# Performance work log

Hardware: AMD Instinct MI355X
Metric: run time of the kernel (lower is better)

The kernel has to match this reference:

```python
import jax, jax.numpy as jnp
import numpy as np

B, C_FEATS, T = 8, 256, 1024
NUM_COMP = 64
EPS = 1e-9


def setup_inputs() -> dict:
    key = jax.random.key(0)
    k1, k2 = jax.random.split(key)
    x = jax.random.normal(k1, (B, C_FEATS, T), dtype=jnp.float32)
    mu = jax.random.normal(k2, (NUM_COMP, C_FEATS), dtype=jnp.float32)
    prec = jnp.ones((NUM_COMP,), dtype=jnp.float32)
    return {"x": x, "mu": mu, "prec": prec}


def reference(x, mu, prec):
    # x: (B, F, T) -> (B, T, F), matching torch transpose(1, -1)
    xt = jnp.swapaxes(x, 1, 2)
    # squared distance to each centroid via expansion (avoids (B,T,C,F) delta):
    x2 = jnp.sum(xt * xt, axis=-1, keepdims=True)            # (B, T, 1)
    mu2 = jnp.sum(mu * mu, axis=-1)                           # (C,)
    xmu = jnp.einsum('btf,cf->btc', xt, mu)                   # (B, T, C)
    dist = x2 - 2.0 * xmu + mu2                               # (B, T, C)
    llk = -(prec * prec) * dist                               # use_bias=False
    r = jax.nn.softmax(llk, axis=-1)                          # (B, T, C)
    Nraw = jnp.sum(r, axis=1)                                 # (B, C)
    N = Nraw + EPS
    # F = sum_t r*(x - mu) = sum_t r*x - (sum_t r)*mu
    F = jnp.einsum('btc,btf->bcf', r, xt) - Nraw[..., None] * mu  # (B, C, F)
    pool = F / N[..., None]
    return pool.reshape(x.shape[0], -1)                       # (B, C*F)
```

## Files before the change

kernel.cpp:

```cpp
#include <hip/hip_runtime.h>

#define BB 8
#define FF 256
#define TT 1024
#define CC 64
constexpr float EPS = 1e-9f;

#define TCHUNK 16
#define NTILE 64
#define BT 64
#define NTQ 16
#define BCF (BB * CC * FF)

#define WS_R   0
#define WS_NP  524288
#define WS_FP  557056

__global__ __launch_bounds__(256) void passA_kernel(const float* __restrict__ x,
                                                    const float* __restrict__ mu,
                                                    const float* __restrict__ prec,
                                                    float* __restrict__ ws) {
    __shared__ __align__(16) float xt[TCHUNK][260];
    __shared__ __align__(16) float Sred[4][TCHUNK][68];
    __shared__ __align__(16) float rl[TCHUNK][68];
    __shared__ float x2s[TCHUNK];
    __shared__ float mu2s[CC], p2s[CC];

    const int tid = threadIdx.x;
    const int b    = blockIdx.x >> 6;
    const int tile = blockIdx.x & 63;
    const int t0   = tile * TCHUNK;
    const float* xb = x + (size_t)b * FF * TT;

    {
        const int c = tid >> 2, q = tid & 3;
        const float* mp = mu + c * FF + q * 64;
        float s = 0.f;
        #pragma unroll
        for (int i = 0; i < 16; ++i) {
            float4 v = *(const float4*)(mp + i * 4);
            s += v.x * v.x + v.y * v.y + v.z * v.z + v.w * v.w;
        }
        s += __shfl_xor(s, 1);
        s += __shfl_xor(s, 2);
        if (q == 0) mu2s[c] = s;
        if (tid < CC) { float p = prec[tid]; p2s[tid] = p * p; }
    }

    #pragma unroll
    for (int i = 0; i < 4; ++i) {
        const int id = i * 256 + tid;
        const int f = id >> 2, seg = id & 3;
        float4 v = *(const float4*)(xb + f * TT + t0 + seg * 4);
        xt[seg * 4 + 0][f] = v.x;
        xt[seg * 4 + 1][f] = v.y;
        xt[seg * 4 + 2][f] = v.z;
        xt[seg * 4 + 3][f] = v.w;
    }
    __syncthreads();

    {
        const int t = tid >> 4, kk = tid & 15;
        float s = 0.f;
        #pragma unroll
        for (int q = 0; q < 16; ++q) { float v = xt[t][kk + 16 * q]; s += v * v; }
        s += __shfl_xor(s, 1);
        s += __shfl_xor(s, 2);
        s += __shfl_xor(s, 4);
        s += __shfl_xor(s, 8);
        if (kk == 0) x2s[t] = s;
    }
    __syncthreads();

    {
        const int g = tid >> 6;
        const int lane = tid & 63;
        const int tr = lane & 7;
        const int c0 = (lane >> 3) * 8;
        float acc[2][8];
        #pragma unroll
        for (int i = 0; i < 2; ++i)
            #pragma unroll
            for (int j = 0; j < 8; ++j) acc[i][j] = 0.f;

        const float* mupt = mu + (size_t)c0 * FF + g * 64;
        #pragma unroll 4
        for (int kk = 0; kk < 16; ++kk) {
            const int f4 = g * 64 + kk * 4;
            float4 xv0 = *(const float4*)&xt[tr][f4];
            float4 xv1 = *(const float4*)&xt[tr + 8][f4];
            #pragma unroll
            for (int j = 0; j < 8; ++j) {
                float4 mv = *(const float4*)(mupt + j * FF + kk * 4);
                acc[0][j] += xv0.x * mv.x + xv0.y * mv.y + xv0.z * mv.z + xv0.w * mv.w;
                acc[1][j] += xv1.x * mv.x + xv1.y * mv.y + xv1.z * mv.z + xv1.w * mv.w;
            }
        }
        #pragma unroll
        for (int i = 0; i < 2; ++i) {
            *(float4*)&Sred[g][tr + 8 * i][c0] =
                make_float4(acc[i][0], acc[i][1], acc[i][2], acc[i][3]);
            *(float4*)&Sred[g][tr + 8 * i][c0 + 4] =
                make_float4(acc[i][4], acc[i][5], acc[i][6], acc[i][7]);
        }
    }
    __syncthreads();

    {
        const int t = tid >> 4, kk = tid & 15;
        const int c4 = kk * 4;
        float Sx = 0.f, Sy = 0.f, Sz = 0.f, Sw = 0.f;
        #pragma unroll
        for (int gg = 0; gg < 4; ++gg) {
            float4 v = *(const float4*)&Sred[gg][t][c4];
            Sx += v.x; Sy += v.y; Sz += v.z; Sw += v.w;
        }
        const float x2v = x2s[t];
        float l0 = -p2s[c4 + 0] * (x2v - 2.f * Sx + mu2s[c4 + 0]);
        float l1 = -p2s[c4 + 1] * (x2v - 2.f * Sy + mu2s[c4 + 1]);
        float l2 = -p2s[c4 + 2] * (x2v - 2.f * Sz + mu2s[c4 + 2]);
        float l3 = -p2s[c4 + 3] * (x2v - 2.f * Sw + mu2s[c4 + 3]);
        float m = fmaxf(fmaxf(l0, l1), fmaxf(l2, l3));
        m = fmaxf(m, __shfl_xor(m, 1));
        m = fmaxf(m, __shfl_xor(m, 2));
        m = fmaxf(m, __shfl_xor(m, 4));
        m = fmaxf(m, __shfl_xor(m, 8));
        float e0 = __expf(l0 - m), e1 = __expf(l1 - m);
        float e2 = __expf(l2 - m), e3 = __expf(l3 - m);
        float sum = e0 + e1 + e2 + e3;
        sum += __shfl_xor(sum, 1);
        sum += __shfl_xor(sum, 2);
        sum += __shfl_xor(sum, 4);
        sum += __shfl_xor(sum, 8);
        const float inv = 1.f / sum;
        *(float4*)&rl[t][c4] = make_float4(e0 * inv, e1 * inv, e2 * inv, e3 * inv);
    }
    __syncthreads();

    if (tid < CC) {
        float ns = 0.f;
        #pragma unroll
        for (int t = 0; t < TCHUNK; ++t) ns += rl[t][tid];
        ws[WS_NP + (size_t)blockIdx.x * CC + tid] = ns;
    }

    {
        const int c = tid >> 2, seg = tid & 3;
        float4 v;
        v.x = rl[seg * 4 + 0][c];
        v.y = rl[seg * 4 + 1][c];
        v.z = rl[seg * 4 + 2][c];
        v.w = rl[seg * 4 + 3][c];
        *(float4*)(ws + WS_R + ((size_t)b * CC + c) * TT + t0 + seg * 4) = v;
    }
}

__global__ __launch_bounds__(256) void passB_kernel(const float* __restrict__ x,
                                                    float* __restrict__ ws) {
    __shared__ __align__(16) float xs[BT][68];
    __shared__ __align__(16) float rs[CC][68];
    const int tid = threadIdx.x;
    const int bid = blockIdx.x;
    const int b   = bid >> 6;
    const int fsl = (bid >> 4) & 3;
    const int tq  = bid & 15;
    const int f0  = fsl * 64;
    const int t0  = tq * BT;
    const float* xb = x + (size_t)b * FF * TT;
    const float* rb = ws + WS_R + (size_t)b * CC * TT;

    #pragma unroll
    for (int it = 0; it < 4; ++it) {
        const int id = it * 256 + tid;
        {
            const int ff = id >> 4, seg = id & 15;
            float4 v = *(const float4*)(xb + (f0 + ff) * TT + t0 + seg * 4);
            xs[seg * 4 + 0][ff] = v.x;
            xs[seg * 4 + 1][ff] = v.y;
            xs[seg * 4 + 2][ff] = v.z;
            xs[seg * 4 + 3][ff] = v.w;
        }
        {
            const int c = id >> 4, cs = id & 15;
            float4 v = *(const float4*)(rb + (size_t)c * TT + t0 + cs * 4);
            *(float4*)&rs[c][cs * 4] = v;
        }
    }
    __syncthreads();

    const int fi = tid & 15, cg = tid >> 4;
    float acc[4][4];
    #pragma unroll
    for (int j = 0; j < 4; ++j)
        #pragma unroll
        for (int e = 0; e < 4; ++e) acc[j][e] = 0.f;

    #pragma unroll 8
    for (int t = 0; t < BT; ++t) {
        float4 xv = *(const float4*)&xs[t][fi * 4];
        #pragma unroll
        for (int j = 0; j < 4; ++j) {
            float rv = rs[cg * 4 + j][t];
            acc[j][0] += rv * xv.x;
            acc[j][1] += rv * xv.y;
            acc[j][2] += rv * xv.z;
            acc[j][3] += rv * xv.w;
        }
    }

    float* fp = ws + WS_FP + (size_t)tq * BCF + (size_t)b * CC * FF;
    #pragma unroll
    for (int j = 0; j < 4; ++j)
        *(float4*)(fp + (cg * 4 + j) * FF + f0 + fi * 4) =
            make_float4(acc[j][0], acc[j][1], acc[j][2], acc[j][3]);
}

__global__ __launch_bounds__(256) void final_kernel(const float* __restrict__ mu,
                                                    const float* __restrict__ ws,
                                                    float* __restrict__ out) {
    const int b = blockIdx.x >> 6, c = blockIdx.x & 63;
    const int f = threadIdx.x;
    float nr = 0.f;
    const float* np = ws + WS_NP + (size_t)b * NTILE * CC + c;
    #pragma unroll
    for (int tile = 0; tile < NTILE; ++tile) nr += np[tile * CC];
    const float* fp = ws + WS_FP + (size_t)b * CC * FF + c * FF + f;
    float s = 0.f;
    #pragma unroll
    for (int p = 0; p < NTQ; ++p) s += fp[(size_t)p * BCF];
    out[((size_t)b * CC + c) * FF + f] = (s - nr * mu[c * FF + f]) / (nr + EPS);
}

extern "C" void kernel_launch(void* const* d_in, const int* in_sizes, int n_in,
                              void* d_out, int out_size, void* d_ws, size_t ws_size,
                              hipStream_t stream) {
    const float* x    = (const float*)d_in[0];
    const float* mu   = (const float*)d_in[1];
    const float* prec = (const float*)d_in[2];
    float* out = (float*)d_out;
    float* ws  = (float*)d_ws;

    passA_kernel<<<512, 256, 0, stream>>>(x, mu, prec, ws);
    passB_kernel<<<512, 256, 0, stream>>>(x, ws);
    final_kernel<<<512, 256, 0, stream>>>(mu, ws, out);
}
```

Baseline: 33.44 us.

## Restructure phase-1 distance GEMV without cross-group reduction; transpose r tile in phase 2

Phase 1 now gives each thread one timestep and four centroids and runs over all 256 features. It computes x^2 inline, which removes the Sred cross-group reduction buffer, the separate x2 pass and two barriers. The cost is that every thread streams its own mu rows from global memory and runs a longer serial loop with less ILP. Phase 2 stores the responsibility tile transposed in shared memory, so the inner loop reads one float4 of r per timestep instead of four scalar loads. This adds strided scalar LDS writes during the fill.

```diff
diff --git a/kernel.cpp b/kernel.cpp
--- a/kernel.cpp
+++ b/kernel.cpp
@@ -6,30 +6,26 @@
 #define CC 64
 constexpr float EPS = 1e-9f;
 
-#define TCHUNK 16
-#define NTILE 64
 #define BT 64
 #define NTQ 16
+#define NTILE 64
 #define BCF (BB * CC * FF)
 
 #define WS_R   0
 #define WS_NP  524288
 #define WS_FP  557056
 
-__global__ __launch_bounds__(256) void passA_kernel(const float* __restrict__ x,
-                                                    const float* __restrict__ mu,
-                                                    const float* __restrict__ prec,
-                                                    float* __restrict__ ws) {
-    __shared__ __align__(16) float xt[TCHUNK][260];
-    __shared__ __align__(16) float Sred[4][TCHUNK][68];
-    __shared__ __align__(16) float rl[TCHUNK][68];
-    __shared__ float x2s[TCHUNK];
+__global__ __launch_bounds__(256, 4) void k_phase1(
+        const float* __restrict__ x, const float* __restrict__ mu,
+        const float* __restrict__ prec, float* __restrict__ ws) {
+    __shared__ __align__(16) float xt[16][260];
+    __shared__ __align__(16) float rl[16][68];
     __shared__ float mu2s[CC], p2s[CC];
 
     const int tid = threadIdx.x;
     const int b    = blockIdx.x >> 6;
     const int tile = blockIdx.x & 63;
-    const int t0   = tile * TCHUNK;
+    const int t0   = tile * 16;
     const float* xb = x + (size_t)b * FF * TT;
 
     {
@@ -48,8 +44,8 @@
     }
 
     #pragma unroll
-    for (int i = 0; i < 4; ++i) {
-        const int id = i * 256 + tid;
+    for (int it = 0; it < 4; ++it) {
+        const int id = it * 256 + tid;
         const int f = id >> 2, seg = id & 3;
         float4 v = *(const float4*)(xb + f * TT + t0 + seg * 4);
         xt[seg * 4 + 0][f] = v.x;
@@ -60,66 +56,28 @@
     __syncthreads();
 
     {
-        const int t = tid >> 4, kk = tid & 15;
-        float s = 0.f;
-        #pragma unroll
-        for (int q = 0; q < 16; ++q) { float v = xt[t][kk + 16 * q]; s += v * v; }
-        s += __shfl_xor(s, 1);
-        s += __shfl_xor(s, 2);
-        s += __shfl_xor(s, 4);
-        s += __shfl_xor(s, 8);
-        if (kk == 0) x2s[t] = s;
-    }
-    __syncthreads();
-
-    {
-        const int g = tid >> 6;
-        const int lane = tid & 63;
-        const int tr = lane & 7;
-        const int c0 = (lane >> 3) * 8;
-        float acc[2][8];
-        #pragma unroll
-        for (int i = 0; i < 2; ++i)
-            #pragma unroll
-            for (int j = 0; j < 8; ++j) acc[i][j] = 0.f;
-
-        const float* mupt = mu + (size_t)c0 * FF + g * 64;
+        const int tc = tid & 15, tg = tid >> 4;
+        const int c4 = tc * 4;
+        float acc0 = 0.f, acc1 = 0.f, acc2 = 0.f, acc3 = 0.f, x2v = 0.f;
+        const float* mup = mu + (size_t)c4 * FF;
         #pragma unroll 4
-        for (int kk = 0; kk < 16; ++kk) {
-            const int f4 = g * 64 + kk * 4;
-            float4 xv0 = *(const float4*)&xt[tr][f4];
-            float4 xv1 = *(const float4*)&xt[tr + 8][f4];
-            #pragma unroll
-            for (int j = 0; j < 8; ++j) {
-                float4 mv = *(const float4*)(mupt + j * FF + kk * 4);
-                acc[0][j] += xv0.x * mv.x + xv0.y * mv.y + xv0.z * mv.z + xv0.w * mv.w;
-                acc[1][j] += xv1.x * mv.x + xv1.y * mv.y + xv1.z * mv.z + xv1.w * mv.w;
-            }
-        }
-        #pragma unroll
-        for (int i = 0; i < 2; ++i) {
-            *(float4*)&Sred[g][tr + 8 * i][c0] =
-                make_float4(acc[i][0], acc[i][1], acc[i][2], acc[i][3]);
-            *(float4*)&Sred[g][tr + 8 * i][c0 + 4] =
-                make_float4(acc[i][4], acc[i][5], acc[i][6], acc[i][7]);
-        }
-    }
-    __syncthreads();
-
-    {
-        const int t = tid >> 4, kk = tid & 15;
-        const int c4 = kk * 4;
-        float Sx = 0.f, Sy = 0.f, Sz = 0.f, Sw = 0.f;
-        #pragma unroll
-        for (int gg = 0; gg < 4; ++gg) {
-            float4 v = *(const float4*)&Sred[gg][t][c4];
-            Sx += v.x; Sy += v.y; Sz += v.z; Sw += v.w;
-        }
-        const float x2v = x2s[t];
-        float l0 = -p2s[c4 + 0] * (x2v - 2.f * Sx + mu2s[c4 + 0]);
-        float l1 = -p2s[c4 + 1] * (x2v - 2.f * Sy + mu2s[c4 + 1]);
-        float l2 = -p2s[c4 + 2] * (x2v - 2.f * Sz + mu2s[c4 + 2]);
-        float l3 = -p2s[c4 + 3] * (x2v - 2.f * Sw + mu2s[c4 + 3]);
+        for (int kk = 0; kk < 64; ++kk) {
+            float4 xv = *(const float4*)&xt[tg][kk * 4];
+            x2v += xv.x * xv.x + xv.y * xv.y + xv.z * xv.z + xv.w * xv.w;
+            float4 m0 = *(const float4*)(mup + 0 * FF + kk * 4);
+            float4 m1 = *(const float4*)(mup + 1 * FF + kk * 4);
+            float4 m2 = *(const float4*)(mup + 2 * FF + kk * 4);
+            float4 m3 = *(const float4*)(mup + 3 * FF + kk * 4);
+            acc0 += xv.x * m0.x + xv.y * m0.y + xv.z * m0.z + xv.w * m0.w;
+            acc1 += xv.x * m1.x + xv.y * m1.y + xv.z * m1.z + xv.w * m1.w;
+            acc2 += xv.x * m2.x + xv.y * m2.y + xv.z * m2.z + xv.w * m2.w;
+            acc3 += xv.x * m3.x + xv.y * m3.y + xv.z * m3.z + xv.w * m3.w;
+        }
+
+        float l0 = -p2s[c4 + 0] * (x2v - 2.f * acc0 + mu2s[c4 + 0]);
+        float l1 = -p2s[c4 + 1] * (x2v - 2.f * acc1 + mu2s[c4 + 1]);
+        float l2 = -p2s[c4 + 2] * (x2v - 2.f * acc2 + mu2s[c4 + 2]);
+        float l3 = -p2s[c4 + 3] * (x2v - 2.f * acc3 + mu2s[c4 + 3]);
         float m = fmaxf(fmaxf(l0, l1), fmaxf(l2, l3));
         m = fmaxf(m, __shfl_xor(m, 1));
         m = fmaxf(m, __shfl_xor(m, 2));
@@ -133,14 +91,14 @@
         sum += __shfl_xor(sum, 4);
         sum += __shfl_xor(sum, 8);
         const float inv = 1.f / sum;
-        *(float4*)&rl[t][c4] = make_float4(e0 * inv, e1 * inv, e2 * inv, e3 * inv);
+        *(float4*)&rl[tg][c4] = make_float4(e0 * inv, e1 * inv, e2 * inv, e3 * inv);
     }
     __syncthreads();
 
     if (tid < CC) {
         float ns = 0.f;
         #pragma unroll
-        for (int t = 0; t < TCHUNK; ++t) ns += rl[t][tid];
+        for (int t = 0; t < 16; ++t) ns += rl[t][tid];
         ws[WS_NP + (size_t)blockIdx.x * CC + tid] = ns;
     }
 
@@ -155,10 +113,10 @@
     }
 }
 
-__global__ __launch_bounds__(256) void passB_kernel(const float* __restrict__ x,
-                                                    float* __restrict__ ws) {
-    __shared__ __align__(16) float xs[BT][68];
-    __shared__ __align__(16) float rs[CC][68];
+__global__ __launch_bounds__(256) void k_phase2(const float* __restrict__ x,
+                                                float* __restrict__ ws) {
+    __shared__ float xs[BT][68];
+    __shared__ float rs[CC][68];
     const int tid = threadIdx.x;
     const int bid = blockIdx.x;
     const int b   = bid >> 6;
@@ -183,7 +141,10 @@
         {
             const int c = id >> 4, cs = id & 15;
             float4 v = *(const float4*)(rb + (size_t)c * TT + t0 + cs * 4);
-            *(float4*)&rs[c][cs * 4] = v;
+            rs[cs * 4 + 0][c] = v.x;
+            rs[cs * 4 + 1][c] = v.y;
+            rs[cs * 4 + 2][c] = v.z;
+            rs[cs * 4 + 3][c] = v.w;
         }
     }
     __syncthreads();
@@ -198,26 +159,27 @@
     #pragma unroll 8
     for (int t = 0; t < BT; ++t) {
         float4 xv = *(const float4*)&xs[t][fi * 4];
-        #pragma unroll
-        for (int j = 0; j < 4; ++j) {
-            float rv = rs[cg * 4 + j][t];
-            acc[j][0] += rv * xv.x;
-            acc[j][1] += rv * xv.y;
-            acc[j][2] += rv * xv.z;
-            acc[j][3] += rv * xv.w;
-        }
+        float4 rv = *(const float4*)&rs[t][cg * 4];
+        acc[0][0] += rv.x * xv.x; acc[0][1] += rv.x * xv.y;
+        acc[0][2] += rv.x * xv.z; acc[0][3] += rv.x * xv.w;
+        acc[1][0] += rv.y * xv.x; acc[1][1] += rv.y * xv.y;
+        acc[1][2] += rv.y * xv.z; acc[1][3] += rv.y * xv.w;
+        acc[2][0] += rv.z * xv.x; acc[2][1] += rv.z * xv.y;
+        acc[2][2] += rv.z * xv.z; acc[2][3] += rv.z * xv.w;
+        acc[3][0] += rv.w * xv.x; acc[3][1] += rv.w * xv.y;
+        acc[3][2] += rv.w * xv.z; acc[3][3] += rv.w * xv.w;
     }
 
     float* fp = ws + WS_FP + (size_t)tq * BCF + (size_t)b * CC * FF;
     #pragma unroll
     for (int j = 0; j < 4; ++j)
-        *(float4*)(fp + (cg * 4 + j) * FF + f0 + fi * 4) =
+        *(float4*)(fp + (size_t)(cg * 4 + j) * FF + f0 + fi * 4) =
             make_float4(acc[j][0], acc[j][1], acc[j][2], acc[j][3]);
 }
 
-__global__ __launch_bounds__(256) void final_kernel(const float* __restrict__ mu,
-                                                    const float* __restrict__ ws,
-                                                    float* __restrict__ out) {
+__global__ __launch_bounds__(256) void k_phase3(const float* __restrict__ mu,
+                                                const float* __restrict__ ws,
+                                                float* __restrict__ out) {
     const int b = blockIdx.x >> 6, c = blockIdx.x & 63;
     const int f = threadIdx.x;
     float nr = 0.f;
@@ -240,7 +202,7 @@
     float* out = (float*)d_out;
     float* ws  = (float*)d_ws;
 
-    passA_kernel<<<512, 256, 0, stream>>>(x, mu, prec, ws);
-    passB_kernel<<<512, 256, 0, stream>>>(x, ws);
-    final_kernel<<<512, 256, 0, stream>>>(mu, ws, out);
-}
+    k_phase1<<<512, 256, 0, stream>>>(x, mu, prec, ws);
+    k_phase2<<<512, 256, 0, stream>>>(x, ws);
+    k_phase3<<<512, 256, 0, stream>>>(mu, ws, out);
+}
```

New measurement: 80.11 us. 2.4x slower.
